# Kernel tuning notes

Measured on AMD Instinct MI355X. Metric: run time of the kernel, lower is better.

The kernel has to match this reference:

```python
import jax, jax.numpy as jnp
import numpy as np


def conv2d(x, w, b, pad):
    # x: [B,Cin,H,W], w: [Cout,Cin,kh,kw]
    y = jax.lax.conv_general_dilated(
        x, w, window_strides=(1, 1), padding=[(pad, pad), (pad, pad)],
        dimension_numbers=('NCHW', 'OIHW', 'NCHW'))
    return y + b[None, :, None, None]


def setup_inputs() -> dict:
    key = jax.random.key(0)
    ks = jax.random.split(key, 11)
    B, C, H, W = 4, 128, 64, 64
    Cc, Hc, Wc = 256, 32, 32
    s = 0.05
    return {
        'sr_feat': jax.random.normal(ks[0], (B, C, H, W), jnp.float32),
        'context_feat': jax.random.normal(ks[1], (B, Cc, Hc, Wc), jnp.float32),
        'Wq': jax.random.normal(ks[2], (C, C, 1, 1), jnp.float32) * s,
        'bq': jax.random.normal(ks[3], (C,), jnp.float32) * s,
        'Wk': jax.random.normal(ks[4], (C, Cc, 1, 1), jnp.float32) * s,
        'bk': jax.random.normal(ks[5], (C,), jnp.float32) * s,
        'Wv': jax.random.normal(ks[6], (C, Cc, 1, 1), jnp.float32) * s,
        'bv': jax.random.normal(ks[7], (C,), jnp.float32) * s,
        'Wp': jax.random.normal(ks[8], (C, C, 3, 3), jnp.float32) * s,
        'bp': jax.random.normal(ks[9], (C,), jnp.float32) * s,
        'gamma': jax.random.normal(ks[10], (1,), jnp.float32) * s,
    }


def reference(sr_feat, context_feat, Wq, bq, Wk, bk, Wv, bv, Wp, bp, gamma):
    B, C, H, W = sr_feat.shape
    Cc = context_feat.shape[1]
    # bilinear upsample (half-pixel centers == align_corners=False)
    ctx = jax.image.resize(context_feat, (B, Cc, H, W), method='bilinear')
    q = conv2d(sr_feat, Wq, bq, 0).reshape(B, C, H * W)   # [B,C,N]
    k = conv2d(ctx, Wk, bk, 0).reshape(B, C, H * W)       # [B,C,N]
    v = conv2d(ctx, Wv, bv, 0).reshape(B, C, H * W)       # [B,C,N]
    # attn[b,n,m] = softmax_m( sum_c q[b,c,n] * k[b,c,m] )
    attn = jax.nn.softmax(jnp.einsum('bcn,bcm->bnm', q, k), axis=-1)
    # out[b,c,n] = sum_m v[b,c,m] * attn[b,n,m]
    out = jnp.einsum('bcm,bnm->bcn', v, attn).reshape(B, C, H, W)
    return sr_feat + gamma[0] * conv2d(out, Wp, bp, 1)
```

## Files before the change

kernel.cpp:

```cpp
#include <hip/hip_runtime.h>
#include <math.h>

#define NB 4
#define C  128
#define CCH 256
#define HH 64
#define WW 64
#define NN 4096
#define NS 1024
#define HC 32
#define WC 32
#define PP 66
#define LOG2E 1.44269504088896f
#define NSPLIT 4

typedef unsigned short u16;
typedef unsigned int uint32;
typedef short s16x8 __attribute__((ext_vector_type(8)));
typedef float f32x4 __attribute__((ext_vector_type(4)));
typedef float f32x16 __attribute__((ext_vector_type(16)));

#if __has_builtin(__builtin_amdgcn_exp2f)
#define EXP2(x) __builtin_amdgcn_exp2f(x)
#else
#define EXP2(x) __expf((x) * 0.69314718056f)
#endif

__device__ __forceinline__ u16 f2bf(float f) {
    uint32 u = __float_as_uint(f);
    u += 0x7fffu + ((u >> 16) & 1u);
    return (u16)(u >> 16);
}
__device__ __forceinline__ float bf2f(u16 h) {
    return __uint_as_float((uint32)h << 16);
}

__global__ __launch_bounds__(256) void prep2(const float* __restrict__ ctx,
                                             const float* __restrict__ sr,
                                             const float* __restrict__ Wq,
                                             const float* __restrict__ Wk,
                                             const float* __restrict__ Wv,
                                             const float* __restrict__ Wp,
                                             u16* __restrict__ ctx_s,
                                             u16* __restrict__ sr_t,
                                             u16* __restrict__ wbf,
                                             u16* __restrict__ wt,
                                             uint4* __restrict__ att_z) {
    __shared__ float ls[64 * 65];
    int blk = blockIdx.x;
    int tid = threadIdx.x;

    if (blk < 256) {
        int idx = blk;
        int n0 = (idx & 15) * 64;
        int ci0 = ((idx >> 4) & 3) * 64;
        int b = idx >> 6;
        const float* inb = ctx + ((size_t)b * CCH + ci0) * NS + n0;
#pragma unroll
        for (int L = 0; L < 4; L++) {
            int fc = tid + L * 256;
            int nc = fc & 15, ci = fc >> 4;
            float4 v = *(const float4*)(inb + (size_t)ci * NS + nc * 4);
            float* d = &ls[ci * 65 + nc * 4];
            d[0] = v.x; d[1] = v.y; d[2] = v.z; d[3] = v.w;
        }
        __syncthreads();
        u16* ob = ctx_s + ((size_t)b * NS + n0) * CCH + ci0;
#pragma unroll
        for (int j = 0; j < 16; j++) {
            int o = tid + j * 256;
            int ci = o & 63, n = o >> 6;
            ob[(size_t)n * CCH + ci] = f2bf(ls[ci * 65 + n]);
        }
    } else if (blk < 768) {
        int idx = blk - 256;
        int n0 = (idx & 63) * 64;
        int ci0 = ((idx >> 6) & 1) * 64;
        int b = idx >> 7;
        const float* inb = sr + ((size_t)b * C + ci0) * NN + n0;
#pragma unroll
        for (int L = 0; L < 4; L++) {
            int fc = tid + L * 256;
            int nc = fc & 15, ci = fc >> 4;
            float4 v = *(const float4*)(inb + (size_t)ci * NN + nc * 4);
            float* d = &ls[ci * 65 + nc * 4];
            d[0] = v.x; d[1] = v.y; d[2] = v.z; d[3] = v.w;
        }
        __syncthreads();
        u16* ob = sr_t + ((size_t)b * NN + n0) * C + ci0;
#pragma unroll
        for (int j = 0; j < 16; j++) {
            int o = tid + j * 256;
            int ci = o & 63, n = o >> 6;
            ob[(size_t)n * C + ci] = f2bf(ls[ci * 65 + n]);
        }
    } else if (blk < 1664) {
        int i = (blk - 768) * 256 + tid;
        if (i < 81920) {
            float v;
            if (i < 16384) v = Wq[i] * LOG2E;
            else if (i < 49152) v = Wk[i - 16384];
            else v = Wv[i - 49152];
            wbf[i] = f2bf(v);
        } else {
            int idx = i - 81920;
            int ciin = idx & 31;
            int co = (idx >> 5) & 127;
            int cb = (idx >> 12) & 3;
            int pos = idx >> 14;
            int ky = pos / 3, kx = pos - ky * 3;
            int ci = cb * 32 + ciin;
            wt[idx] = f2bf(Wp[((size_t)(co * C + ci) * 3 + ky) * 3 + kx]);
        }
    } else {
        int i = (blk - 1664) * 256 + tid;
        if (i < 278784) att_z[i] = make_uint4(0, 0, 0, 0);
    }
}

__global__ __launch_bounds__(256) void proj_all2(const u16* __restrict__ sr_t,
                                                 const u16* __restrict__ ctx_s,
                                                 const u16* __restrict__ wbf,
                                                 const float* __restrict__ bq,
                                                 const float* __restrict__ bk,
                                                 const float* __restrict__ bv,
                                                 u16* __restrict__ q_t,
                                                 u16* __restrict__ k_s,
                                                 u16* __restrict__ v_s) {
    __shared__ u16 xs[128 * 64];
    __shared__ u16 wsm[2][128 * 64];
    int b = blockIdx.y;
    int tid = threadIdx.x;
    int w = tid >> 6, lane = tid & 63, l31 = lane & 31, half = lane >> 5;
    int xh = w >> 1, wh = w & 1;

    if (blockIdx.x < 32) {
        int n0 = blockIdx.x * 128;
        const u16* xb = sr_t + (size_t)b * NN * C;
        f32x16 acc[2][2];
#pragma unroll
        for (int xt = 0; xt < 2; xt++)
#pragma unroll
            for (int wt2 = 0; wt2 < 2; wt2++)
#pragma unroll
                for (int i = 0; i < 16; i++) acc[xt][wt2][i] = 0.f;
        for (int c0i = 0; c0i < 2; c0i++) {
            int c0 = c0i * 64;
            __syncthreads();
#pragma unroll
            for (int t = 0; t < 4; t++) {
                int CI = t * 256 + tid;
                int row = CI >> 3, sl = CI & 7;
                int lc = sl ^ (row & 7);
                __builtin_amdgcn_global_load_lds(
                    (const __attribute__((address_space(1))) void*)(xb + (size_t)(n0 + row) * C + c0 + lc * 8),
                    (__attribute__((address_space(3))) void*)&xs[(size_t)CI * 8], 16, 0, 0);
            }
#pragma unroll
            for (int t = 0; t < 4; t++) {
                int CI = t * 256 + tid;
                int co = CI >> 3, sl = CI & 7;
                int lc = sl ^ (co & 7);
                __builtin_amdgcn_global_load_lds(
                    (const __attribute__((address_space(1))) void*)(wbf + (size_t)co * C + c0 + lc * 8),
                    (__attribute__((address_space(3))) void*)&wsm[0][(size_t)CI * 8], 16, 0, 0);
            }
            __syncthreads();
#pragma unroll
            for (int kg = 0; kg < 4; kg++) {
                int pc = ((kg * 2 + half) ^ (l31 & 7)) * 8;
                s16x8 xf[2], wf2[2];
#pragma unroll
                for (int xt = 0; xt < 2; xt++)
                    xf[xt] = *(const s16x8*)&xs[(xh * 64 + xt * 32 + l31) * 64 + pc];
#pragma unroll
                for (int wt2 = 0; wt2 < 2; wt2++)
                    wf2[wt2] = *(const s16x8*)&wsm[0][(wh * 64 + wt2 * 32 + l31) * 64 + pc];
#pragma unroll
                for (int xt = 0; xt < 2; xt++)
#pragma unroll
                    for (int wt2 = 0; wt2 < 2; wt2++)
                        acc[xt][wt2] = __builtin_amdgcn_mfma_f32_32x32x16_bf16(xf[xt], wf2[wt2], acc[xt][wt2], 0, 0, 0);
            }
        }
        u16* ot = q_t + (size_t)b * NN * C;
        float bv2[2];
#pragma unroll
        for (int wt2 = 0; wt2 < 2; wt2++) bv2[wt2] = bq[wh * 64 + wt2 * 32 + l31] * LOG2E;
#pragma unroll
        for (int xt = 0; xt < 2; xt++)
#pragma unroll
            for (int r = 0; r < 16; r++) {
                int n = n0 + xh * 64 + xt * 32 + (r & 3) + 8 * (r >> 2) + 4 * half;
#pragma unroll
                for (int wt2 = 0; wt2 < 2; wt2++)
                    ot[(size_t)n * C + wh * 64 + wt2 * 32 + l31] = f2bf(acc[xt][wt2][r] + bv2[wt2]);
            }
    } else {
        int n0 = (blockIdx.x - 32) * 64;
        const u16* xb = ctx_s + (size_t)b * NS * CCH;
        const u16* wkb = wbf + 16384;
        const u16* wvb = wbf + 49152;
        f32x16 acck[2], accv[2];
#pragma unroll
        for (int wt2 = 0; wt2 < 2; wt2++)
#pragma unroll
            for (int i = 0; i < 16; i++) { acck[wt2][i] = 0.f; accv[wt2][i] = 0.f; }
        for (int c0i = 0; c0i < 4; c0i++) {
            int c0 = c0i * 64;
            __syncthreads();
#pragma unroll
            for (int t = 0; t < 2; t++) {
                int CI = t * 256 + tid;
                int row = CI >> 3, sl = CI & 7;
                int lc = sl ^ (row & 7);
                __builtin_amdgcn_global_load_lds(
                    (const __attribute__((address_space(1))) void*)(xb + (size_t)(n0 + row) * CCH + c0 + lc * 8),
                    (__attribute__((address_space(3))) void*)&xs[(size_t)CI * 8], 16, 0, 0);
            }
#pragma unroll
            for (int t = 0; t < 4; t++) {
                int CI = t * 256 + tid;
                int co = CI >> 3, sl = CI & 7;
                int lc = sl ^ (co & 7);
                __builtin_amdgcn_global_load_lds(
                    (const __attribute__((address_space(1))) void*)(wkb + (size_t)co * CCH + c0 + lc * 8),
                    (__attribute__((address_space(3))) void*)&wsm[0][(size_t)CI * 8], 16, 0, 0);
            }
#pragma unroll
            for (int t = 0; t < 4; t++) {
                int CI = t * 256 + tid;
                int co = CI >> 3, sl = CI & 7;
                int lc = sl ^ (co & 7);
                __builtin_amdgcn_global_load_lds(
                    (const __attribute__((address_space(1))) void*)(wvb + (size_t)co * CCH + c0 + lc * 8),
                    (__attribute__((address_space(3))) void*)&wsm[1][(size_t)CI * 8], 16, 0, 0);
            }
            __syncthreads();
#pragma unroll
            for (int kg = 0; kg < 4; kg++) {
                int pc = ((kg * 2 + half) ^ (l31 & 7)) * 8;
                s16x8 xf = *(const s16x8*)&xs[(xh * 32 + l31) * 64 + pc];
                s16x8 wfk[2], wfv[2];
#pragma unroll
                for (int wt2 = 0; wt2 < 2; wt2++) {
                    wfk[wt2] = *(const s16x8*)&wsm[0][(wh * 64 + wt2 * 32 + l31) * 64 + pc];
                    wfv[wt2] = *(const s16x8*)&wsm[1][(wh * 64 + wt2 * 32 + l31) * 64 + pc];
                }
#pragma unroll
                for (int wt2 = 0; wt2 < 2; wt2++) {
                    acck[wt2] = __builtin_amdgcn_mfma_f32_32x32x16_bf16(xf, wfk[wt2], acck[wt2], 0, 0, 0);
                    accv[wt2] = __builtin_amdgcn_mfma_f32_32x32x16_bf16(wfv[wt2], xf, accv[wt2], 0, 0, 0);
                }
            }
        }
        u16* ok = k_s + (size_t)b * NS * C;
#pragma unroll
        for (int wt2 = 0; wt2 < 2; wt2++) {
            float bvk = bk[wh * 64 + wt2 * 32 + l31];
#pragma unroll
            for (int r = 0; r < 16; r++) {
                int n = n0 + xh * 32 + (r & 3) + 8 * (r >> 2) + 4 * half;
                ok[(size_t)n * C + wh * 64 + wt2 * 32 + l31] = f2bf(acck[wt2][r] + bvk);
            }
        }
        u16* ov = v_s + (size_t)b * C * NS;
#pragma unroll
        for (int wt2 = 0; wt2 < 2; wt2++)
#pragma unroll
            for (int r = 0; r < 16; r++) {
                int co = wh * 64 + wt2 * 32 + (r & 3) + 8 * (r >> 2) + 4 * half;
                ov[(size_t)co * NS + n0 + xh * 32 + l31] = f2bf(accv[wt2][r] + bv[co]);
            }
    }
}

__global__ __launch_bounds__(256) void upsample_v(const u16* __restrict__ v_s,
                                                  u16* __restrict__ v_bf) {
    __shared__ u16 lsv[NS];
    int idx = blockIdx.x;
    int tid = threadIdx.x;
    int c = idx & 127, b = idx >> 7;
    const u16* vp = v_s + ((size_t)b * C + c) * NS;
    if (tid < 128) *(uint4*)&lsv[tid * 8] = *(const uint4*)(vp + tid * 8);
    __syncthreads();
    u16* ob = v_bf + ((size_t)b * C + c) * NN;
#pragma unroll
    for (int j = 0; j < 16; j++) {
        int n = tid + j * 256;
        int y = n >> 6, x = n & 63;
        float sy = y * 0.5f - 0.25f;
        float sx = x * 0.5f - 0.25f;
        int y0 = (int)floorf(sy), x0 = (int)floorf(sx);
        float wy = sy - (float)y0, wx = sx - (float)x0;
        int y0c = y0 < 0 ? 0 : y0;
        int y1c = (y0 + 1 > HC - 1) ? HC - 1 : y0 + 1;
        int x0c = x0 < 0 ? 0 : x0;
        int x1c = (x0 + 1 > WC - 1) ? WC - 1 : x0 + 1;
        float v00 = bf2f(lsv[y0c * WC + x0c]), v01 = bf2f(lsv[y0c * WC + x1c]);
        float v10 = bf2f(lsv[y1c * WC + x0c]), v11 = bf2f(lsv[y1c * WC + x1c]);
        ob[n] = f2bf((1.f - wy) * ((1.f - wx) * v00 + wx * v01)
                   +        wy  * ((1.f - wx) * v10 + wx * v11));
    }
}

__global__ __launch_bounds__(256, 3) void flash_mfma(const u16* __restrict__ qt_p,
                                                     const u16* __restrict__ ks_p,
                                                     const u16* __restrict__ vt_p,
                                                     u16* __restrict__ part,
                                                     float* __restrict__ lpart) {
    __shared__ u16 ksr[2][32 * 128];
    __shared__ u16 vs[2][128 * 64];

    int ib = blockIdx.x;
    int b = (ib & 7) >> 1;
    int rest = ((ib >> 3) << 1) | (ib & 1);
    int qtile = rest >> 2;
    int split = rest & 3;
    int n0 = qtile * 128;
    int tid = threadIdx.x;
    int w = tid >> 6, lane = tid & 63, l31 = lane & 31, half = lane >> 5;

    const u16* qtb = qt_p + (size_t)b * NN * C;
    const u16* ksb = ks_p + (size_t)b * NS * C;
    const u16* vtb = vt_p + (size_t)b * C * NN;

    auto stageKrow = [&](int buf, int r) {
#pragma unroll
        for (int t = 0; t < 2; t++) {
            int CI = t * 256 + tid;
            int row = CI >> 4;
            int lc = (CI & 15) ^ (row & 15);
            __builtin_amdgcn_global_load_lds(
                (const __attribute__((address_space(1))) void*)(ksb + (size_t)(r * 32 + row) * C + lc * 8),
                (__attribute__((address_space(3))) void*)&ksr[buf][(size_t)CI * 8], 16, 0, 0);
        }
    };
    auto stageV = [&](int buf, int m0) {
#pragma unroll
        for (int t = 0; t < 4; t++) {
            int CI = (w * 4 + t) * 64 + lane;
            int c = CI >> 3;
            int lc = (CI & 7) ^ (c & 7);
            __builtin_amdgcn_global_load_lds(
                (const __attribute__((address_space(1))) void*)(vtb + (size_t)c * NN + m0 + lc * 8),
                (__attribute__((address_space(3))) void*)&vs[buf][(w * 4 + t) * 512], 16, 0, 0);
        }
    };

    int qrow = n0 + w * 32 + l31;
    s16x8 qf[8];
#pragma unroll
    for (int kg = 0; kg < 8; kg++)
        qf[kg] = *(const s16x8*)(qtb + (size_t)qrow * C + kg * 16 + half * 8);

    auto scoreTile = [&](int buf) {
        f32x16 st;
#pragma unroll
        for (int i = 0; i < 16; i++) st[i] = 0.f;
        const u16* kb = &ksr[buf][0];
#pragma unroll
        for (int kg = 0; kg < 8; kg++) {
            int pc = ((kg * 2 + half) ^ (l31 & 15)) * 8;
            s16x8 kf = *(const s16x8*)&kb[l31 * 128 + pc];
            st = __builtin_amdgcn_mfma_f32_32x32x16_bf16(kf, qf[kg], st, 0, 0, 0);
        }
        return st;
    };

    int m_base = split * 1024;
    int j0 = split * 8;

    stageKrow(0, split == 0 ? 0 : j0 - 1);
    stageKrow(1, j0);
    stageV(0, m_base);
    __syncthreads();
    f32x16 sA = scoreTile(0);
    f32x16 sB = scoreTile(1);
    __syncthreads();

    f32x16 oacc[4];
#pragma unroll
    for (int mt = 0; mt < 4; mt++)
#pragma unroll
        for (int i = 0; i < 16; i++) oacc[mt][i] = 0.f;
    float lsum = 0.f;

#pragma unroll 2
    for (int it = 0; it < 16; it++) {
        int buf = it & 1;
        int m0 = m_base + it * 64;
        if (it < 15) stageV(buf ^ 1, m0 + 64);
        if ((it & 1) == 0) {
            int rs = j0 + 1 + (it >> 1);
            if (rs <= 31) stageKrow((it >> 1) & 1, rs);
        } else {
            sA = sB;
            int rn = j0 + 1 + (it >> 1);
            if (rn <= 31) sB = scoreTile((it >> 1) & 1);
        }

        float wB = (it & 1) ? 0.25f : 0.75f;
        float wA = 1.0f - wB;
        float cc[16];
#pragma unroll
        for (int i = 0; i < 16; i++) cc[i] = wA * sA[i] + wB * sB[i];

        float xr0  = __shfl_xor(cc[0], 32);
        float xr3  = __shfl_xor(cc[3], 32);
        float xr4  = __shfl_xor(cc[4], 32);
        float xr7  = __shfl_xor(cc[7], 32);
        float xr8  = __shfl_xor(cc[8], 32);
        float xr11 = __shfl_xor(cc[11], 32);
        float xr12 = __shfl_xor(cc[12], 32);
        float xr15 = __shfl_xor(cc[15], 32);
        float d0s[4], d5s[4];
        d0s[0] = half ? xr3  : cc[0];
        d0s[1] = half ? xr7  : xr3;
        d0s[2] = half ? xr11 : xr7;
        d0s[3] = half ? xr15 : xr11;
        d5s[0] = half ? xr4  : xr0;
        d5s[1] = half ? xr8  : xr4;
        d5s[2] = half ? xr12 : xr8;
        d5s[3] = half ? cc[15] : xr12;

        const u16* vsb = &vs[buf][0];
#pragma unroll
        for (int s = 0; s < 4; s++) {
            float d0 = d0s[s], d1 = cc[4 * s], d2 = cc[4 * s + 1];
            float d3 = cc[4 * s + 2], d4 = cc[4 * s + 3], d5 = d5s[s];
            float e1 = 0.75f * d1, e2 = 0.75f * d2, e3 = 0.75f * d3, e4 = 0.75f * d4;
            float p0 = EXP2(fmaf(0.25f, d0, e1));
            float p1 = EXP2(fmaf(0.25f, d2, e1));
            float p2 = EXP2(fmaf(0.25f, d1, e2));
            float p3 = EXP2(fmaf(0.25f, d3, e2));
            float p4 = EXP2(fmaf(0.25f, d2, e3));
            float p5 = EXP2(fmaf(0.25f, d4, e3));
            float p6 = EXP2(fmaf(0.25f, d3, e4));
            float p7 = EXP2(fmaf(0.25f, d5, e4));
            lsum += ((p0 + p1) + (p2 + p3)) + ((p4 + p5) + (p6 + p7));
            union { uint32 u[4]; s16x8 v; } pu;
            pu.u[0] = __builtin_amdgcn_perm(__float_as_uint(p1), __float_as_uint(p0), 0x07060302u);
            pu.u[1] = __builtin_amdgcn_perm(__float_as_uint(p3), __float_as_uint(p2), 0x07060302u);
            pu.u[2] = __builtin_amdgcn_perm(__float_as_uint(p5), __float_as_uint(p4), 0x07060302u);
            pu.u[3] = __builtin_amdgcn_perm(__float_as_uint(p7), __float_as_uint(p6), 0x07060302u);
            int pcv = ((s * 2 + half) ^ (l31 & 7)) * 8;
#pragma unroll
            for (int mt = 0; mt < 4; mt++) {
                s16x8 vf = *(const s16x8*)&vsb[(mt * 32 + l31) * 64 + pcv];
                oacc[mt] = __builtin_amdgcn_mfma_f32_32x32x16_bf16(vf, pu.v, oacc[mt], 0, 0, 0);
            }
        }
        __syncthreads();
    }

    float lt = lsum + __shfl_xor(lsum, 32);
    if (half == 0) lpart[(size_t)split * NB * NN + (size_t)b * NN + qrow] = lt;
    u16* pb = part + ((size_t)split * NB + b) * (size_t)C * NN;
#pragma unroll
    for (int mt = 0; mt < 4; mt++)
#pragma unroll
        for (int r = 0; r < 16; r++) {
            int c = mt * 32 + (r & 3) + 8 * (r >> 2) + 4 * half;
            pb[(size_t)c * NN + n0 + w * 32 + l31] = f2bf(oacc[mt][r]);
        }
}

__global__ __launch_bounds__(256) void flash_combine(const u16* __restrict__ part,
                                                     const float* __restrict__ lpart,
                                                     u16* __restrict__ att_t) {
    __shared__ u16 ts[128 * 66];
    __shared__ float linv[64];
    int b = blockIdx.y;
    int nt = blockIdx.x;
    int n0 = nt * 64;
    int tid = threadIdx.x;
    if (tid < 64) {
        float s = 0.f;
#pragma unroll
        for (int sp = 0; sp < NSPLIT; sp++)
            s += lpart[(size_t)sp * NB * NN + (size_t)b * NN + n0 + tid];
        linv[tid] = 1.0f / s;
    }
    __syncthreads();
#pragma unroll
    for (int j = 0; j < 32; j++) {
        int e = tid + j * 256;
        int n = e & 63, c = e >> 6;
        float o = 0.f;
#pragma unroll
        for (int sp = 0; sp < NSPLIT; sp++)
            o += bf2f(part[((size_t)sp * NB + b) * (size_t)C * NN + (size_t)c * NN + n0 + n]);
        ts[c * 66 + n] = f2bf(o * linv[n]);
    }
    __syncthreads();
    u16* ob = att_t + ((size_t)b * PP * PP + (size_t)(nt + 1) * PP + 1) * C;
#pragma unroll
    for (int j = 0; j < 32; j++) {
        int o = tid + j * 256;
        int c = o & 127, n = o >> 7;
        ob[(size_t)n * C + c] = ts[c * 66 + n];
    }
}

__global__ __launch_bounds__(256) void conv3x3_mfma(const u16* __restrict__ att_t,
                                                    const u16* __restrict__ wt,
                                                    const float* __restrict__ bp,
                                                    const float* __restrict__ sr,
                                                    const float* __restrict__ gamma,
                                                    float* __restrict__ out) {
    __shared__ u16 in_s[2][4 * 102 * 8];
    int ib = blockIdx.x;
    int b = (ib & 7) >> 1;
    int rr = ((ib >> 3) << 1) | (ib & 1);
    int y = rr >> 1;
    int x0 = (rr & 1) * 32;
    int tid = threadIdx.x;
    int w = tid >> 6, lane = tid & 63, l = tid & 15, quad = (tid >> 4) & 3;
    const u16* ab = att_t + (size_t)b * (PP * PP * C);

    auto stage = [&](int cib, int bufi) {
        u16* base = &in_s[bufi][w * 102 * 8];
        const u16* gsrc = ab + cib * 32 + w * 8;
#pragma unroll
        for (int t = 0; t < 2; t++) {
            int idx = t * 64 + lane;
            int r = idx / 34, xp = idx - r * 34;
            if (t == 0 || lane < 38)
                __builtin_amdgcn_global_load_lds(
                    (const __attribute__((address_space(1))) void*)(gsrc + (size_t)((y + r) * PP + x0 + xp) * C),
                    (__attribute__((address_space(3))) void*)(base + (size_t)t * 64 * 8), 16, 0, 0);
        }
    };

    f32x4 accr[2][2];
#pragma unroll
    for (int cf = 0; cf < 2; cf++)
#pragma unroll
        for (int nf = 0; nf < 2; nf++) accr[cf][nf] = (f32x4){0.f, 0.f, 0.f, 0.f};
    int cow = w * 32;

    stage(0, 0);
    __syncthreads();
#pragma unroll
    for (int cib = 0; cib < 4; cib++) {
        if (cib < 3) stage(cib + 1, (cib + 1) & 1);
        s16x8 wf[9][2];
#pragma unroll
        for (int pos = 0; pos < 9; pos++)
#pragma unroll
            for (int cf = 0; cf < 2; cf++)
                wf[pos][cf] = *(const s16x8*)&wt[((size_t)(pos * 4 + cib) * C + cow + cf * 16 + l) * 32 + quad * 8];
        const u16* bufc = &in_s[cib & 1][0];
#pragma unroll
        for (int ky = 0; ky < 3; ky++)
#pragma unroll
            for (int kx = 0; kx < 3; kx++) {
                int pos = ky * 3 + kx;
#pragma unroll
                for (int nf = 0; nf < 2; nf++) {
                    s16x8 inf = *(const s16x8*)&bufc[(quad * 102 + ky * 34 + nf * 16 + l + kx) * 8];
                    accr[0][nf] = __builtin_amdgcn_mfma_f32_16x16x32_bf16(wf[pos][0], inf, accr[0][nf], 0, 0, 0);
                    accr[1][nf] = __builtin_amdgcn_mfma_f32_16x16x32_bf16(wf[pos][1], inf, accr[1][nf], 0, 0, 0);
                }
            }
        __syncthreads();
    }

    float g = gamma[0];
    float* ob = out + (size_t)b * C * NN;
    const float* sb = sr + (size_t)b * C * NN;
#pragma unroll
    for (int cf = 0; cf < 2; cf++)
#pragma unroll
        for (int r = 0; r < 4; r++) {
            int co = cow + cf * 16 + quad * 4 + r;
            float bias = bp[co];
#pragma unroll
            for (int nf = 0; nf < 2; nf++) {
                size_t oo = (size_t)co * NN + y * 64 + x0 + nf * 16 + l;
                ob[oo] = sb[oo] + g * (accr[cf][nf][r] + bias);
            }
        }
}

extern "C" void kernel_launch(void* const* d_in, const int* in_sizes, int n_in,
                              void* d_out, int out_size, void* d_ws, size_t ws_size,
                              hipStream_t stream) {
    const float* sr    = (const float*)d_in[0];
    const float* ctx   = (const float*)d_in[1];
    const float* Wq    = (const float*)d_in[2];
    const float* bq    = (const float*)d_in[3];
    const float* Wk    = (const float*)d_in[4];
    const float* bk    = (const float*)d_in[5];
    const float* Wv    = (const float*)d_in[6];
    const float* bv    = (const float*)d_in[7];
    const float* Wp    = (const float*)d_in[8];
    const float* bp    = (const float*)d_in[9];
    const float* gamma = (const float*)d_in[10];
    float* out = (float*)d_out;

    char* wsb = (char*)d_ws;
    u16*   att_t  = (u16*)wsb;
    u16*   part   = (u16*)(wsb + (5u << 20));
    float* lpart  = (float*)(wsb + (21u << 20));
    u16*   ctx_s  = (u16*)(wsb + (22u << 20));
    u16*   sr_t   = (u16*)(wsb + (25u << 20));
    u16*   q_t    = (u16*)(wsb + (29u << 20));
    u16*   k_s    = (u16*)(wsb + (33u << 20));
    u16*   v_s    = (u16*)(wsb + (34u << 20));
    u16*   v_bf   = (u16*)(wsb + (39u << 20));
    u16*   wt     = (u16*)(wsb + (43u << 20));
    u16*   w_bf   = (u16*)(wsb + (43u << 20) + (512u << 10));

    prep2<<<dim3(2753), 256, 0, stream>>>(ctx, sr, Wq, Wk, Wv, Wp,
                                          ctx_s, sr_t, w_bf, wt, (uint4*)att_t);
    proj_all2<<<dim3(48, NB), 256, 0, stream>>>(sr_t, ctx_s, w_bf, bq, bk, bv,
                                                q_t, k_s, v_s);
    upsample_v<<<dim3(512), 256, 0, stream>>>(v_s, v_bf);
    flash_mfma<<<dim3(512), 256, 0, stream>>>(q_t, k_s, v_bf, part, lpart);
    flash_combine<<<dim3(64, NB), 256, 0, stream>>>(part, lpart, att_t);
    conv3x3_mfma<<<dim3(512), 256, 0, stream>>>(att_t, wt, bp, sr, gamma, out);
}
```

Baseline: 172.4 us.

## Split flash attention over eight key ranges and prefetch K scores earlier

```diff
diff --git a/kernel.cpp b/kernel.cpp
--- a/kernel.cpp
+++ b/kernel.cpp
@@ -12,7 +12,7 @@
 #define WC 32
 #define PP 66
 #define LOG2E 1.44269504088896f
-#define NSPLIT 4
+#define NSPLIT 8
 
 typedef unsigned short u16;
 typedef unsigned int uint32;
@@ -313,10 +313,9 @@
     __shared__ u16 vs[2][128 * 64];
 
     int ib = blockIdx.x;
-    int b = (ib & 7) >> 1;
-    int rest = ((ib >> 3) << 1) | (ib & 1);
-    int qtile = rest >> 2;
-    int split = rest & 3;
+    int split = ib & 7;
+    int b = (ib >> 3) & 3;
+    int qtile = ib >> 5;
     int n0 = qtile * 128;
     int tid = threadIdx.x;
     int w = tid >> 6, lane = tid & 63, l31 = lane & 31, half = lane >> 5;
@@ -368,8 +367,8 @@
         return st;
     };
 
-    int m_base = split * 1024;
-    int j0 = split * 8;
+    int m_base = split * 512;
+    int j0 = split * 4;
 
     stageKrow(0, split == 0 ? 0 : j0 - 1);
     stageKrow(1, j0);
@@ -378,7 +377,10 @@
     f32x16 sA = scoreTile(0);
     f32x16 sB = scoreTile(1);
     __syncthreads();
-
+    stageKrow(0, j0 + 1);
+    __syncthreads();
+
+    f32x16 sC;
     f32x16 oacc[4];
 #pragma unroll
     for (int mt = 0; mt < 4; mt++)
@@ -387,17 +389,20 @@
     float lsum = 0.f;
 
 #pragma unroll 2
-    for (int it = 0; it < 16; it++) {
+    for (int it = 0; it < 8; it++) {
         int buf = it & 1;
         int m0 = m_base + it * 64;
-        if (it < 15) stageV(buf ^ 1, m0 + 64);
+        if (it < 7) stageV(buf ^ 1, m0 + 64);
         if ((it & 1) == 0) {
-            int rs = j0 + 1 + (it >> 1);
-            if (rs <= 31) stageKrow((it >> 1) & 1, rs);
+            int rn = j0 + 1 + (it >> 1);
+            if (rn <= 31) sC = scoreTile((it >> 1) & 1);
         } else {
+            int u = it >> 1;
+            int rs = j0 + 2 + u;
+            if (rs <= 31) stageKrow((u + 1) & 1, rs);
             sA = sB;
-            int rn = j0 + 1 + (it >> 1);
-            if (rn <= 31) sB = scoreTile((it >> 1) & 1);
+            int rn = j0 + 1 + u;
+            if (rn <= 31) sB = sC;
         }
 
         float wB = (it & 1) ? 0.25f : 0.75f;
@@ -602,23 +607,23 @@
 
     char* wsb = (char*)d_ws;
     u16*   att_t  = (u16*)wsb;
-    u16*   part   = (u16*)(wsb + (5u << 20));
-    float* lpart  = (float*)(wsb + (21u << 20));
-    u16*   ctx_s  = (u16*)(wsb + (22u << 20));
-    u16*   sr_t   = (u16*)(wsb + (25u << 20));
-    u16*   q_t    = (u16*)(wsb + (29u << 20));
-    u16*   k_s    = (u16*)(wsb + (33u << 20));
-    u16*   v_s    = (u16*)(wsb + (34u << 20));
-    u16*   v_bf   = (u16*)(wsb + (39u << 20));
-    u16*   wt     = (u16*)(wsb + (43u << 20));
-    u16*   w_bf   = (u16*)(wsb + (43u << 20) + (512u << 10));
+    u16*   part   = (u16*)(wsb + (4u << 20) + (512u << 10));
+    u16*   ctx_s  = (u16*)(wsb + (4u << 20) + (512u << 10));
+    u16*   sr_t   = (u16*)(wsb + (6u << 20) + (512u << 10));
+    u16*   v_s    = (u16*)(wsb + (10u << 20) + (512u << 10));
+    u16*   q_t    = (u16*)(wsb + (36u << 20) + (512u << 10));
+    u16*   k_s    = (u16*)(wsb + (40u << 20) + (512u << 10));
+    u16*   v_bf   = (u16*)(wsb + (41u << 20) + (512u << 10));
+    float* lpart  = (float*)(wsb + (45u << 20) + (512u << 10));
+    u16*   wt     = (u16*)(wsb + (46u << 20));
+    u16*   w_bf   = (u16*)(wsb + (46u << 20) + (512u << 10));
 
     prep2<<<dim3(2753), 256, 0, stream>>>(ctx, sr, Wq, Wk, Wv, Wp,
                                           ctx_s, sr_t, w_bf, wt, (uint4*)att_t);
     proj_all2<<<dim3(48, NB), 256, 0, stream>>>(sr_t, ctx_s, w_bf, bq, bk, bv,
                                                 q_t, k_s, v_s);
     upsample_v<<<dim3(512), 256, 0, stream>>>(v_s, v_bf);
-    flash_mfma<<<dim3(512), 256, 0, stream>>>(q_t, k_s, v_bf, part, lpart);
+    flash_mfma<<<dim3(1024), 256, 0, stream>>>(q_t, k_s, v_bf, part, lpart);
     flash_combine<<<dim3(64, NB), 256, 0, stream>>>(part, lpart, att_t);
     conv3x3_mfma<<<dim3(512), 256, 0, stream>>>(att_t, wt, bp, sr, gamma, out);
 }
```

Result: slower. 195.6 us (+13.5%).
